# Optimization experiments

Measured on AMD Instinct MI355X. Metric: run time of the kernel, lower is better.

## Reference

```python
import jax, jax.numpy as jnp
import numpy as np

FIELD_DIMS = [40000] * 26
OUTPUT_DIM = 1
FEATURE_DIM = int(np.sum(FIELD_DIMS))  # 1_040_000
BATCH = 65536
NUM_FIELDS = len(FIELD_DIMS)


def setup_inputs() -> dict:
    key = jax.random.key(0)
    kx, kw = jax.random.split(key)
    # per-field indices in [0, field_dim)
    x = jax.random.randint(kx, (BATCH, NUM_FIELDS), 0, 40000, dtype=jnp.int64 if jax.config.jax_enable_x64 else jnp.int32)
    # offsets: start of each field in the flattened feature space
    offsets = jnp.asarray(np.concatenate([[0], np.cumsum(FIELD_DIMS)[:-1]]), dtype=x.dtype)
    # nn.Linear weight is (output_dim, feature_dim); store transposed for gather: (feature_dim, output_dim)
    W = 0.01 * jax.random.normal(kw, (FEATURE_DIM, OUTPUT_DIM), dtype=jnp.float32)
    b = jnp.zeros((OUTPUT_DIM,), dtype=jnp.float32)
    return {"x": x, "offsets": offsets, "W": W, "b": b}


def reference(x, offsets, W, b):
    # one-hot scatter + dense Linear == gather rows of W at offset-adjusted ids and sum over fields
    idx = x + offsets[None, :]            # (B, F)
    rows = W[idx]                          # (B, F, output_dim)
    return rows.sum(axis=1) + b            # (B, output_dim)
```

## Files before the change

kernel.cpp:

```cpp
#include <hip/hip_runtime.h>
#include <hip/hip_bf16.h>


#define NUM_FIELDS 26

__global__ __launch_bounds__(256) void FeaturesLinear_kernel(
    const int* __restrict__ x,
    const int* __restrict__ offsets,
    const float* __restrict__ W,
    const float* __restrict__ bias,
    float* __restrict__ out,
    int batch) {
  const int l = threadIdx.x & 31;
  const int row = (blockIdx.x * blockDim.x + threadIdx.x) >> 5;
  if (row >= batch) return;

  const int lc = (l < NUM_FIELDS) ? l : (NUM_FIELDS - 1);
  const int idx = x[row * NUM_FIELDS + lc] + offsets[lc];
  float v = W[idx];
  if (l >= NUM_FIELDS) v = 0.f;

#pragma unroll
  for (int m = 16; m > 0; m >>= 1) v += __shfl_xor(v, m, 32);

  if (l == 0) out[row] = v + bias[0];
}

extern "C" void kernel_launch(void* const* d_in, const int* in_sizes, int n_in,
                              void* d_out, int out_size, void* d_ws, size_t ws_size,
                              hipStream_t stream) {
  const int* x = (const int*)d_in[0];
  const int* offsets = (const int*)d_in[1];
  const float* W = (const float*)d_in[2];
  const float* bias = (const float*)d_in[3];
  float* out = (float*)d_out;

  int batch = in_sizes[0] / NUM_FIELDS;

  const int block = 256;
  const int rows_per_block = block / 32;
  dim3 grid((batch + rows_per_block - 1) / rows_per_block);
  FeaturesLinear_kernel<<<grid, dim3(block), 0, stream>>>(x, offsets, W, bias, out, batch);
}
```

Baseline: 75.88 us.

## Stage indices in shared memory and process four rows per 32-lane group

Each block now copies its whole contiguous slab of x into LDS with coalesced loads. Each 32-lane group then handles four batch rows, issuing four independent W gathers per lane before doing interleaved shuffle reductions. The goal is to improve index-load coalescing and add memory-level parallelism for the random W gathers, while cutting the block count by a factor of four. The launch drops the tail bounds check, so it assumes batch is a multiple of 32 rows, and it adds an LDS barrier.

```diff
diff --git a/kernel.cpp b/kernel.cpp
--- a/kernel.cpp
+++ b/kernel.cpp
@@ -3,6 +3,11 @@
 
 
 #define NUM_FIELDS 26
+#define ROWS_PER_GROUP 4
+#define BLOCK 256
+#define GROUPS_PER_BLOCK (BLOCK / 32)
+#define ROWS_PER_BLOCK (GROUPS_PER_BLOCK * ROWS_PER_GROUP)
+#define INTS_PER_BLOCK (ROWS_PER_BLOCK * NUM_FIELDS)
 
 __global__ __launch_bounds__(256) void FeaturesLinear_kernel(
     const int* __restrict__ x,
@@ -11,19 +16,46 @@
     const float* __restrict__ bias,
     float* __restrict__ out,
     int batch) {
-  const int l = threadIdx.x & 31;
-  const int row = (blockIdx.x * blockDim.x + threadIdx.x) >> 5;
-  if (row >= batch) return;
+  __shared__ int xs[INTS_PER_BLOCK];
 
-  const int lc = (l < NUM_FIELDS) ? l : (NUM_FIELDS - 1);
-  const int idx = x[row * NUM_FIELDS + lc] + offsets[lc];
-  float v = W[idx];
-  if (l >= NUM_FIELDS) v = 0.f;
+  const int tid = threadIdx.x;
+  const int block_row0 = blockIdx.x * ROWS_PER_BLOCK;
+  const int* xb = x + block_row0 * NUM_FIELDS;
 
 #pragma unroll
-  for (int m = 16; m > 0; m >>= 1) v += __shfl_xor(v, m, 32);
+  for (int i = 0; i < (INTS_PER_BLOCK + BLOCK - 1) / BLOCK; ++i) {
+    int o = tid + i * BLOCK;
+    if (o < INTS_PER_BLOCK) xs[o] = xb[o];
+  }
+  __syncthreads();
 
-  if (l == 0) out[row] = v + bias[0];
+  const int l = tid & 31;
+  const int g = tid >> 5;
+  const int lc = (l < NUM_FIELDS) ? l : (NUM_FIELDS - 1);
+  const int off = offsets[lc];
+
+  int idx[ROWS_PER_GROUP];
+#pragma unroll
+  for (int r = 0; r < ROWS_PER_GROUP; ++r) {
+    idx[r] = xs[(g * ROWS_PER_GROUP + r) * NUM_FIELDS + lc] + off;
+  }
+  float v[ROWS_PER_GROUP];
+#pragma unroll
+  for (int r = 0; r < ROWS_PER_GROUP; ++r) {
+    float t = W[idx[r]];
+    v[r] = (l < NUM_FIELDS) ? t : 0.f;
+  }
+
+#pragma unroll
+  for (int m = 16; m > 0; m >>= 1) {
+#pragma unroll
+    for (int r = 0; r < ROWS_PER_GROUP; ++r) v[r] += __shfl_xor(v[r], m, 32);
+  }
+
+  if (l < ROWS_PER_GROUP) {
+    float wv = (l == 0) ? v[0] : (l == 1) ? v[1] : (l == 2) ? v[2] : v[3];
+    out[block_row0 + g * ROWS_PER_GROUP + l] = wv + bias[0];
+  }
 }
 
 extern "C" void kernel_launch(void* const* d_in, const int* in_sizes, int n_in,
@@ -37,8 +69,6 @@
 
   int batch = in_sizes[0] / NUM_FIELDS;
 
-  const int block = 256;
-  const int rows_per_block = block / 32;
-  dim3 grid((batch + rows_per_block - 1) / rows_per_block);
-  FeaturesLinear_kernel<<<grid, dim3(block), 0, stream>>>(x, offsets, W, bias, out, batch);
+  dim3 grid(batch / ROWS_PER_BLOCK);
+  FeaturesLinear_kernel<<<grid, dim3(BLOCK), 0, stream>>>(x, offsets, W, bias, out, batch);
 }
```

New measurement: 74.89 us. No clear change (-1.3%).
